# Performance work log

Hardware: AMD Instinct MI355X
Metric: run time of the kernel (lower is better)

The kernel has to match this reference:

```python
import jax, jax.numpy as jnp
import numpy as np

D_MODEL, N_HEADS = 512, 8
HEAD_DIM = D_MODEL // N_HEADS
LN_EPS = 1e-5


def setup_inputs() -> dict:
    key = jax.random.key(0)
    ks = jax.random.split(key, 6)
    b, n = 8, 1024
    x = jax.random.normal(ks[0], (b, n, D_MODEL), dtype=jnp.float32)
    W_qkv = jax.random.normal(ks[1], (D_MODEL, 3 * D_MODEL), dtype=jnp.float32) * (1.0 / np.sqrt(D_MODEL))
    b_qkv = jnp.zeros((3 * D_MODEL,), dtype=jnp.float32)
    reattn_w = jax.random.normal(ks[2], (N_HEADS, N_HEADS), dtype=jnp.float32)
    ln_g = jnp.ones((N_HEADS,), dtype=jnp.float32)
    ln_b = jnp.zeros((N_HEADS,), dtype=jnp.float32)
    W_out = jax.random.normal(ks[3], (D_MODEL, D_MODEL), dtype=jnp.float32) * (1.0 / np.sqrt(D_MODEL))
    b_out = jnp.zeros((D_MODEL,), dtype=jnp.float32)
    return {"x": x, "W_qkv": W_qkv, "b_qkv": b_qkv, "reattn_w": reattn_w,
            "ln_g": ln_g, "ln_b": ln_b, "W_out": W_out, "b_out": b_out}


def reference(x, W_qkv, b_qkv, reattn_w, ln_g, ln_b, W_out, b_out):
    b, n, _ = x.shape
    scale = jnp.float32(HEAD_DIM ** -0.5)  # lsa=False -> non-trainable constant
    qkv = x @ W_qkv + b_qkv                                  # (b, n, 3*d_model)
    q, k, v = jnp.split(qkv, 3, axis=-1)
    def to_heads(t):  # b n (h d) -> b h n d
        return t.reshape(b, n, N_HEADS, HEAD_DIM).transpose(0, 2, 1, 3)
    q, k, v = to_heads(q), to_heads(k), to_heads(v)
    scores = jnp.einsum('bhid,bhjd->bhij', q, k) * scale      # (b, h, n, n)
    attn = jax.nn.softmax(scores, axis=-1)
    # cross-head re-attention mix
    attn = jnp.einsum('bhij,hk->bkij', attn, reattn_w)
    # LayerNorm over the head axis (axis=1)
    mu = jnp.mean(attn, axis=1, keepdims=True)
    var = jnp.var(attn, axis=1, keepdims=True)
    attn = (attn - mu) * jax.lax.rsqrt(var + LN_EPS)
    attn = attn * ln_g[None, :, None, None] + ln_b[None, :, None, None]
    out = jnp.einsum('bhij,bhjd->bhid', attn, v)              # (b, h, n, d)
    out = out.transpose(0, 2, 1, 3).reshape(b, n, D_MODEL)    # b n (h d)
    out = out @ W_out + b_out
    return (out, attn)
```

## Files before the change

### kernel.cpp

```cpp
#include <hip/hip_runtime.h>
#include <hip/hip_bf16.h>

#define SCALE_ 0.125f
#define LN_EPS_ 1e-5f

typedef __attribute__((ext_vector_type(8))) short bf16x8;
typedef __attribute__((ext_vector_type(4))) float f32x4;

__device__ __forceinline__ ushort f2b(float f) {
  union { float f; unsigned u; } x; x.f = f;
  unsigned r = x.u + 0x7FFFu + ((x.u >> 16) & 1u);
  return (ushort)(r >> 16);
}
__device__ __forceinline__ unsigned cvtpk(float lo, float hi) {
  union { __hip_bfloat162 h; unsigned u; } x;
  x.h = __float22bfloat162_rn(make_float2(lo, hi));
  return x.u;
}

__device__ __forceinline__ f32x4 mfma16(bf16x8 a, bf16x8 b, f32x4 c) {
  return __builtin_amdgcn_mfma_f32_16x16x32_bf16(a, b, c, 0, 0, 0);
}

__device__ __forceinline__ void bar_lds() {
  asm volatile("s_waitcnt lgkmcnt(0)\n\ts_barrier" ::: "memory");
  __builtin_amdgcn_sched_barrier(0);
}

__global__ __launch_bounds__(256) void cast_transpose(const float* __restrict__ src,
                                                      ushort* __restrict__ dst,
                                                      int R, int C) {
  __shared__ ushort t[64][65];
  const int tid = threadIdx.x;
  const int c0 = blockIdx.x * 64, r0 = blockIdx.y * 64;
  const int lr = tid >> 2, lc = (tid & 3) * 16;
#pragma unroll
  for (int u = 0; u < 4; ++u) {
    float4 v = *(const float4*)&src[(size_t)(r0 + lr) * C + c0 + lc + u * 4];
    t[lc + u * 4 + 0][lr] = f2b(v.x);
    t[lc + u * 4 + 1][lr] = f2b(v.y);
    t[lc + u * 4 + 2][lr] = f2b(v.z);
    t[lc + u * 4 + 3][lr] = f2b(v.w);
  }
  __syncthreads();
#pragma unroll
  for (int u = 0; u < 2; ++u) {
    bf16x8 o;
#pragma unroll
    for (int e = 0; e < 8; ++e) o[e] = (short)t[lr][lc + u * 8 + e];
    *(bf16x8*)&dst[(size_t)(c0 + lr) * R + r0 + lc + u * 8] = o;
  }
}

__global__ __launch_bounds__(256) void qkv_mfma(const float* __restrict__ x,
                                                const ushort* __restrict__ Wt,
                                                const float* __restrict__ bias,
                                                ushort* __restrict__ q,
                                                ushort* __restrict__ k,
                                                ushort* __restrict__ vt) {
  __shared__ ushort A[128][40];
  __shared__ ushort Bs[128][40];
  const int tid = threadIdx.x;
  const int n0 = blockIdx.x * 128;
  const int m0 = blockIdx.y * 128;
  const int lane = tid & 63, wid = tid >> 6;
  const int wr = wid >> 1, wc = wid & 1;
  const int lr = lane & 15, g4 = lane >> 4;
  const int sr = tid >> 1, sco = (tid & 1) * 16;
  f32x4 acc[4][4] = {};
  for (int k0 = 0; k0 < 512; k0 += 32) {
    {
      const float4* xs = (const float4*)&x[(size_t)(m0 + sr) * 512 + k0 + sco];
      float4 v0 = xs[0], v1 = xs[1], v2 = xs[2], v3 = xs[3];
      bf16x8 p0, p1;
      p0[0] = (short)f2b(v0.x); p0[1] = (short)f2b(v0.y);
      p0[2] = (short)f2b(v0.z); p0[3] = (short)f2b(v0.w);
      p0[4] = (short)f2b(v1.x); p0[5] = (short)f2b(v1.y);
      p0[6] = (short)f2b(v1.z); p0[7] = (short)f2b(v1.w);
      p1[0] = (short)f2b(v2.x); p1[1] = (short)f2b(v2.y);
      p1[2] = (short)f2b(v2.z); p1[3] = (short)f2b(v2.w);
      p1[4] = (short)f2b(v3.x); p1[5] = (short)f2b(v3.y);
      p1[6] = (short)f2b(v3.z); p1[7] = (short)f2b(v3.w);
      *(bf16x8*)&A[sr][sco] = p0;
      *(bf16x8*)&A[sr][sco + 8] = p1;
    }
    {
      const bf16x8* wp = (const bf16x8*)&Wt[(size_t)(n0 + sr) * 512 + k0 + sco];
      *(bf16x8*)&Bs[sr][sco] = wp[0];
      *(bf16x8*)&Bs[sr][sco + 8] = wp[1];
    }
    __syncthreads();
    bf16x8 af[4], bf[4];
#pragma unroll
    for (int mr = 0; mr < 4; ++mr) af[mr] = *(bf16x8*)&A[wr * 64 + mr * 16 + lr][g4 * 8];
#pragma unroll
    for (int nr = 0; nr < 4; ++nr) bf[nr] = *(bf16x8*)&Bs[wc * 64 + nr * 16 + lr][g4 * 8];
#pragma unroll
    for (int mr = 0; mr < 4; ++mr)
#pragma unroll
      for (int nr = 0; nr < 4; ++nr) acc[mr][nr] = mfma16(af[mr], bf[nr], acc[mr][nr]);
    __syncthreads();
  }
  const int part = n0 >> 9;
#pragma unroll
  for (int mr = 0; mr < 4; ++mr)
#pragma unroll
    for (int nr = 0; nr < 4; ++nr) {
      const int n = n0 + wc * 64 + nr * 16 + lr;
      const int h = (n & 511) >> 6, d = n & 63;
      const float bb = bias[n];
#pragma unroll
      for (int r = 0; r < 4; ++r) {
        int token = m0 + wr * 64 + mr * 16 + g4 * 4 + r;
        int bi = token >> 10, ii = token & 1023;
        ushort valb = f2b(acc[mr][nr][r] + bb);
        if (part == 0)
          q[(((size_t)(bi * 8 + h) * 1024 + ii) * 64) + d] = valb;
        else if (part == 1)
          k[(((size_t)(bi * 8 + h) * 1024 + ii) * 64) + d] = valb;
        else
          vt[((size_t)(bi * 8 + h) * 64 + d) * 1024 + ii] = valb;
      }
    }
}

__global__ __launch_bounds__(512, 2) void attn_fused(const ushort* __restrict__ q,
                                                     const ushort* __restrict__ k,
                                                     const ushort* __restrict__ vt,
                                                     const float* __restrict__ rw,
                                                     const float* __restrict__ ln_g,
                                                     const float* __restrict__ ln_b,
                                                     float* __restrict__ attn,
                                                     ushort* __restrict__ pv) {
  __shared__ float PM[8][32][36];
  __shared__ float wsh[64];
  __shared__ float gsh[8], bsh[8];

  const int tid = threadIdx.x;
  const int lane = tid & 63;
  const int h = tid >> 6;
  const int obid = ((blockIdx.x & 7) << 5) + (blockIdx.x >> 3);
  const int i0 = (obid & 31) * 32;
  const int b = obid >> 5;
  const int lr = lane & 15, g4 = lane >> 4;

  const int bh = b * 8 + h;
  const ushort* qh = q + ((size_t)bh * 1024 + i0) * 64;
  const ushort* kh = k + (size_t)bh * 65536;
  const ushort* vth = vt + (size_t)bh * 65536;

  if (tid < 64) wsh[tid] = rw[tid];
  if (tid < 8) { gsh[tid] = ln_g[tid]; bsh[tid] = ln_b[tid]; }

  bf16x8 qf[2][2];
#pragma unroll
  for (int ir = 0; ir < 2; ++ir)
#pragma unroll
    for (int ks = 0; ks < 2; ++ks)
      qf[ir][ks] = *(const bf16x8*)&qh[(size_t)(ir * 16 + lr) * 64 + ks * 32 + g4 * 8];

  float psum[2] = {0.f, 0.f};
  {
    bf16x8 kc[4], kn[4];
#pragma unroll
    for (int jr = 0; jr < 2; ++jr)
#pragma unroll
      for (int ks = 0; ks < 2; ++ks)
        kc[jr * 2 + ks] = *(const bf16x8*)&kh[(size_t)(jr * 16 + lr) * 64 + ks * 32 + g4 * 8];
    for (int jt = 0; jt < 32; ++jt) {
      const int j0n = ((jt + 1) & 31) * 32;
#pragma unroll
      for (int jr = 0; jr < 2; ++jr)
#pragma unroll
        for (int ks = 0; ks < 2; ++ks)
          kn[jr * 2 + ks] =
              *(const bf16x8*)&kh[(size_t)(j0n + jr * 16 + lr) * 64 + ks * 32 + g4 * 8];
      f32x4 sa[2][2] = {};
#pragma unroll
      for (int jr = 0; jr < 2; ++jr)
#pragma unroll
        for (int ir = 0; ir < 2; ++ir) {
          sa[jr][ir] = mfma16(kc[jr * 2 + 0], qf[ir][0], sa[jr][ir]);
          sa[jr][ir] = mfma16(kc[jr * 2 + 1], qf[ir][1], sa[jr][ir]);
        }
#pragma unroll
      for (int jr = 0; jr < 2; ++jr)
#pragma unroll
        for (int ir = 0; ir < 2; ++ir)
#pragma unroll
          for (int r = 0; r < 4; ++r) psum[ir] += __expf(sa[jr][ir][r] * SCALE_);
#pragma unroll
      for (int i = 0; i < 4; ++i) kc[i] = kn[i];
    }
  }
  float inv_[2];
#pragma unroll
  for (int ir = 0; ir < 2; ++ir) {
    float s = psum[ir];
    s += __shfl_xor(s, 16);
    s += __shfl_xor(s, 32);
    inv_[ir] = 1.0f / s;
  }

  f32x4 oaccT[4][2] = {};
  const int pair = tid & 1, chunk = tid >> 1;
  const int m_ii = chunk >> 3, m_jj = (chunk & 7) * 4;
  const int k2base = pair * 4;

  bf16x8 kc[4], kn[4];
#pragma unroll
  for (int jr = 0; jr < 2; ++jr)
#pragma unroll
    for (int ks = 0; ks < 2; ++ks)
      kc[jr * 2 + ks] = *(const bf16x8*)&kh[(size_t)(jr * 16 + lr) * 64 + ks * 32 + g4 * 8];

  for (int jt = 0; jt < 32; ++jt) {
    const int j0 = jt * 32;
    const int j0n = ((jt + 1) & 31) * 32;
#pragma unroll
    for (int jr = 0; jr < 2; ++jr)
#pragma unroll
      for (int ks = 0; ks < 2; ++ks)
        kn[jr * 2 + ks] =
            *(const bf16x8*)&kh[(size_t)(j0n + jr * 16 + lr) * 64 + ks * 32 + g4 * 8];

    f32x4 sa[2][2] = {};
#pragma unroll
    for (int jr = 0; jr < 2; ++jr)
#pragma unroll
      for (int ir = 0; ir < 2; ++ir) {
        sa[jr][ir] = mfma16(kc[jr * 2 + 0], qf[ir][0], sa[jr][ir]);
        sa[jr][ir] = mfma16(kc[jr * 2 + 1], qf[ir][1], sa[jr][ir]);
      }
#pragma unroll
    for (int jr = 0; jr < 2; ++jr)
#pragma unroll
      for (int ir = 0; ir < 2; ++ir) {
        f32x4 pw;
#pragma unroll
        for (int r = 0; r < 4; ++r) pw[r] = __expf(sa[jr][ir][r] * SCALE_) * inv_[ir];
        *(f32x4*)&PM[h][ir * 16 + lr][jr * 16 + g4 * 4] = pw;
      }

    bf16x8 vc[4];
#pragma unroll
    for (int dr = 0; dr < 4; ++dr)
      vc[dr] = *(const bf16x8*)&vth[(size_t)(dr * 16 + lr) * 1024 + j0 + g4 * 8];

    bar_lds();

    float4 ph[8];
#pragma unroll
    for (int h2 = 0; h2 < 8; ++h2) ph[h2] = *(const float4*)&PM[h2][m_ii][m_jj];
    float mixed[4][4];
#pragma unroll
    for (int k2l = 0; k2l < 4; ++k2l) {
      float a0 = 0.f, a1 = 0.f, a2 = 0.f, a3 = 0.f;
#pragma unroll
      for (int h2 = 0; h2 < 8; ++h2) {
        float w = wsh[h2 * 8 + k2base + k2l];
        a0 += ph[h2].x * w; a1 += ph[h2].y * w;
        a2 += ph[h2].z * w; a3 += ph[h2].w * w;
      }
      mixed[k2l][0] = a0; mixed[k2l][1] = a1; mixed[k2l][2] = a2; mixed[k2l][3] = a3;
    }
    float mu[4], rs_[4];
#pragma unroll
    for (int e = 0; e < 4; ++e) {
      float mp = mixed[0][e] + mixed[1][e] + mixed[2][e] + mixed[3][e];
      mu[e] = (mp + __shfl_xor(mp, 1)) * 0.125f;
    }
#pragma unroll
    for (int e = 0; e < 4; ++e) {
      float vp = 0.f;
#pragma unroll
      for (int k2l = 0; k2l < 4; ++k2l) {
        float d = mixed[k2l][e] - mu[e];
        vp += d * d;
      }
      float var = (vp + __shfl_xor(vp, 1)) * 0.125f;
      rs_[e] = rsqrtf(var + LN_EPS_);
    }
#pragma unroll
    for (int k2l = 0; k2l < 4; ++k2l) {
      int k2 = k2base + k2l;
      float g = gsh[k2], be = bsh[k2];
      f32x4 o;
      o[0] = (mixed[k2l][0] - mu[0]) * rs_[0] * g + be;
      o[1] = (mixed[k2l][1] - mu[1]) * rs_[1] * g + be;
      o[2] = (mixed[k2l][2] - mu[2]) * rs_[2] * g + be;
      o[3] = (mixed[k2l][3] - mu[3]) * rs_[3] * g + be;
      __builtin_nontemporal_store(
          o, (f32x4*)&attn[((size_t)(b * 8 + k2) << 20) + ((size_t)(i0 + m_ii) << 10) +
                           j0 + m_jj]);
      *(f32x4*)&PM[k2][m_ii][m_jj] = o;
    }

    bar_lds();

    bf16x8 pab[2];
#pragma unroll
    for (int ic = 0; ic < 2; ++ic) {
      const float* pr = &PM[h][ic * 16 + lr][g4 * 8];
      float4 p0 = *(const float4*)&pr[0];
      float4 p1 = *(const float4*)&pr[4];
      union { bf16x8 v; unsigned u[4]; } pk;
      pk.u[0] = cvtpk(p0.x, p0.y);
      pk.u[1] = cvtpk(p0.z, p0.w);
      pk.u[2] = cvtpk(p1.x, p1.y);
      pk.u[3] = cvtpk(p1.z, p1.w);
      pab[ic] = pk.v;
    }
#pragma unroll
    for (int dr = 0; dr < 4; ++dr) {
      oaccT[dr][0] = mfma16(vc[dr], pab[0], oaccT[dr][0]);
      oaccT[dr][1] = mfma16(vc[dr], pab[1], oaccT[dr][1]);
    }

#pragma unroll
    for (int i = 0; i < 4; ++i) kc[i] = kn[i];
  }

  ushort* po = pv + ((size_t)bh * 1024 + i0) * 64;
#pragma unroll
  for (int ic = 0; ic < 2; ++ic)
#pragma unroll
    for (int dr = 0; dr < 4; ++dr) {
      union { ushort4 s; unsigned u[2]; } o;
      o.u[0] = cvtpk(oaccT[dr][ic][0], oaccT[dr][ic][1]);
      o.u[1] = cvtpk(oaccT[dr][ic][2], oaccT[dr][ic][3]);
      *(ushort4*)&po[(size_t)(ic * 16 + lr) * 64 + dr * 16 + g4 * 4] = o.s;
    }
}

__global__ __launch_bounds__(256) void out_mfma(const ushort* __restrict__ pvb,
                                                const ushort* __restrict__ Wt,
                                                const float* __restrict__ bias,
                                                float* __restrict__ out) {
  __shared__ ushort A[128][40];
  __shared__ ushort Bs[128][40];
  const int tid = threadIdx.x;
  const int n0 = blockIdx.x * 128;
  const int m0 = blockIdx.y * 128;
  const int lane = tid & 63, wid = tid >> 6;
  const int wr = wid >> 1, wc = wid & 1;
  const int lr = lane & 15, g4 = lane >> 4;
  const int sr = tid >> 1, sco = (tid & 1) * 16;
  f32x4 acc[4][4] = {};
  for (int k0 = 0; k0 < 512; k0 += 32) {
    {
      int token = m0 + sr;
      int bi = token >> 10, ii = token & 1023;
      int f = k0 + sco;
      int hh = f >> 6, d = f & 63;
      const bf16x8* src =
          (const bf16x8*)&pvb[(((size_t)(bi * 8 + hh)) * 1024 + ii) * 64 + d];
      *(bf16x8*)&A[sr][sco] = src[0];
      *(bf16x8*)&A[sr][sco + 8] = src[1];
    }
    {
      const bf16x8* wp = (const bf16x8*)&Wt[(size_t)(n0 + sr) * 512 + k0 + sco];
      *(bf16x8*)&Bs[sr][sco] = wp[0];
      *(bf16x8*)&Bs[sr][sco + 8] = wp[1];
    }
    __syncthreads();
    bf16x8 af[4], bf[4];
#pragma unroll
    for (int mr = 0; mr < 4; ++mr) af[mr] = *(bf16x8*)&A[wr * 64 + mr * 16 + lr][g4 * 8];
#pragma unroll
    for (int nr = 0; nr < 4; ++nr) bf[nr] = *(bf16x8*)&Bs[wc * 64 + nr * 16 + lr][g4 * 8];
#pragma unroll
    for (int mr = 0; mr < 4; ++mr)
#pragma unroll
      for (int nr = 0; nr < 4; ++nr) acc[mr][nr] = mfma16(af[mr], bf[nr], acc[mr][nr]);
    __syncthreads();
  }
#pragma unroll
  for (int mr = 0; mr < 4; ++mr)
#pragma unroll
    for (int nr = 0; nr < 4; ++nr) {
      const int n = n0 + wc * 64 + nr * 16 + lr;
      const float bb = bias[n];
#pragma unroll
      for (int r = 0; r < 4; ++r) {
        int token = m0 + wr * 64 + mr * 16 + g4 * 4 + r;
        out[(size_t)token * 512 + n] = acc[mr][nr][r] + bb;
      }
    }
}

extern "C" void kernel_launch(void* const* d_in, const int* in_sizes, int n_in,
                              void* d_out, int out_size, void* d_ws, size_t ws_size,
                              hipStream_t stream) {
  const float* x    = (const float*)d_in[0];
  const float* Wqkv = (const float*)d_in[1];
  const float* bqkv = (const float*)d_in[2];
  const float* rw   = (const float*)d_in[3];
  const float* lng  = (const float*)d_in[4];
  const float* lnb  = (const float*)d_in[5];
  const float* Wout = (const float*)d_in[6];
  const float* bout = (const float*)d_in[7];

  float* out  = (float*)d_out;
  float* attn = (float*)d_out + 4194304;

  char* wsb = (char*)d_ws;
  ushort* q     = (ushort*)(wsb);
  ushort* k     = (ushort*)(wsb + (8u << 20));
  ushort* vt    = (ushort*)(wsb + (16u << 20));
  ushort* pvb   = (ushort*)(wsb + (24u << 20));
  ushort* Wqkvt = (ushort*)(wsb + (32u << 20));
  ushort* Woutt = (ushort*)(wsb + (33u << 20) + (1u << 19));

  cast_transpose<<<dim3(24, 8), 256, 0, stream>>>(Wqkv, Wqkvt, 512, 1536);
  cast_transpose<<<dim3(8, 8), 256, 0, stream>>>(Wout, Woutt, 512, 512);

  qkv_mfma<<<dim3(12, 64), 256, 0, stream>>>(x, Wqkvt, bqkv, q, k, vt);
  attn_fused<<<dim3(256), 512, 0, stream>>>(q, k, vt, rw, lng, lnb, attn, pvb);
  out_mfma<<<dim3(4, 64), 256, 0, stream>>>(pvb, Woutt, bout, out);
}
```

Measured before the change: 185.0 us.

## Double-buffer LDS score tiles to drop one barrier per attention step

The shared score/mix buffer is split into two halves, and the loop is software-pipelined. Each iteration computes scores for tile jt into one buffer while the PV matmul for tile jt-1 reads the other, leaving one LDS barrier per iteration instead of two. The aim is to cut block-wide sync stalls and let MFMA work overlap the mixing and LayerNorm phase. It doubles LDS use for this buffer, which could lower occupancy, and adds a prologue and epilogue.

```diff
diff --git a/kernel.cpp b/kernel.cpp
--- a/kernel.cpp
+++ b/kernel.cpp
@@ -132,7 +132,7 @@
                                                      const float* __restrict__ ln_b,
                                                      float* __restrict__ attn,
                                                      ushort* __restrict__ pv) {
-  __shared__ float PM[8][32][36];
+  __shared__ float PMraw[2][8][32][36];
   __shared__ float wsh[64];
   __shared__ float gsh[8], bsh[8];
 
@@ -161,27 +161,27 @@
 
   float psum[2] = {0.f, 0.f};
   {
-    bf16x8 kc[4], kn[4];
+    bf16x8 kc0[4], kn0[4];
 #pragma unroll
     for (int jr = 0; jr < 2; ++jr)
 #pragma unroll
       for (int ks = 0; ks < 2; ++ks)
-        kc[jr * 2 + ks] = *(const bf16x8*)&kh[(size_t)(jr * 16 + lr) * 64 + ks * 32 + g4 * 8];
+        kc0[jr * 2 + ks] = *(const bf16x8*)&kh[(size_t)(jr * 16 + lr) * 64 + ks * 32 + g4 * 8];
     for (int jt = 0; jt < 32; ++jt) {
       const int j0n = ((jt + 1) & 31) * 32;
 #pragma unroll
       for (int jr = 0; jr < 2; ++jr)
 #pragma unroll
         for (int ks = 0; ks < 2; ++ks)
-          kn[jr * 2 + ks] =
+          kn0[jr * 2 + ks] =
               *(const bf16x8*)&kh[(size_t)(j0n + jr * 16 + lr) * 64 + ks * 32 + g4 * 8];
       f32x4 sa[2][2] = {};
 #pragma unroll
       for (int jr = 0; jr < 2; ++jr)
 #pragma unroll
         for (int ir = 0; ir < 2; ++ir) {
-          sa[jr][ir] = mfma16(kc[jr * 2 + 0], qf[ir][0], sa[jr][ir]);
-          sa[jr][ir] = mfma16(kc[jr * 2 + 1], qf[ir][1], sa[jr][ir]);
+          sa[jr][ir] = mfma16(kc0[jr * 2 + 0], qf[ir][0], sa[jr][ir]);
+          sa[jr][ir] = mfma16(kc0[jr * 2 + 1], qf[ir][1], sa[jr][ir]);
         }
 #pragma unroll
       for (int jr = 0; jr < 2; ++jr)
@@ -190,7 +190,7 @@
 #pragma unroll
           for (int r = 0; r < 4; ++r) psum[ir] += __expf(sa[jr][ir][r] * SCALE_);
 #pragma unroll
-      for (int i = 0; i < 4; ++i) kc[i] = kn[i];
+      for (int i = 0; i < 4; ++i) kc0[i] = kn0[i];
     }
   }
   float inv_[2];
@@ -202,6 +202,10 @@
     inv_[ir] = 1.0f / s;
   }
 
+  typedef float pmhead[32][36];
+  pmhead* PS = (pmhead*)PMraw[0];
+  pmhead* PP = (pmhead*)PMraw[1];
+
   f32x4 oaccT[4][2] = {};
   const int pair = tid & 1, chunk = tid >> 1;
   const int m_ii = chunk >> 3, m_jj = (chunk & 7) * 4;
@@ -214,111 +218,119 @@
     for (int ks = 0; ks < 2; ++ks)
       kc[jr * 2 + ks] = *(const bf16x8*)&kh[(size_t)(jr * 16 + lr) * 64 + ks * 32 + g4 * 8];
 
-  for (int jt = 0; jt < 32; ++jt) {
+#define S_PHASE(JT)                                                                   \
+  {                                                                                   \
+    const int j0n_ = (((JT) + 1) & 31) * 32;                                          \
+    _Pragma("unroll") for (int jr = 0; jr < 2; ++jr)                                  \
+        _Pragma("unroll") for (int ks = 0; ks < 2; ++ks)                              \
+            kn[jr * 2 + ks] = *(const bf16x8*)&kh[(size_t)(j0n_ + jr * 16 + lr) * 64 + \
+                                                  ks * 32 + g4 * 8];                  \
+    f32x4 sa[2][2] = {};                                                              \
+    _Pragma("unroll") for (int jr = 0; jr < 2; ++jr)                                  \
+        _Pragma("unroll") for (int ir = 0; ir < 2; ++ir) {                            \
+      sa[jr][ir] = mfma16(kc[jr * 2 + 0], qf[ir][0], sa[jr][ir]);                     \
+      sa[jr][ir] = mfma16(kc[jr * 2 + 1], qf[ir][1], sa[jr][ir]);                     \
+    }                                                                                 \
+    _Pragma("unroll") for (int jr = 0; jr < 2; ++jr)                                  \
+        _Pragma("unroll") for (int ir = 0; ir < 2; ++ir) {                            \
+      f32x4 pw;                                                                       \
+      _Pragma("unroll") for (int r = 0; r < 4; ++r)                                   \
+          pw[r] = __expf(sa[jr][ir][r] * SCALE_) * inv_[ir];                          \
+      *(f32x4*)&PS[h][ir * 16 + lr][jr * 16 + g4 * 4] = pw;                           \
+    }                                                                                 \
+    _Pragma("unroll") for (int i = 0; i < 4; ++i) kc[i] = kn[i];                      \
+  }
+
+#define MIX_PHASE(J0)                                                                 \
+  {                                                                                   \
+    float4 ph[8];                                                                     \
+    _Pragma("unroll") for (int h2 = 0; h2 < 8; ++h2)                                  \
+        ph[h2] = *(const float4*)&PS[h2][m_ii][m_jj];                                 \
+    float mixed[4][4];                                                                \
+    _Pragma("unroll") for (int k2l = 0; k2l < 4; ++k2l) {                             \
+      float a0 = 0.f, a1 = 0.f, a2 = 0.f, a3 = 0.f;                                   \
+      _Pragma("unroll") for (int h2 = 0; h2 < 8; ++h2) {                              \
+        float w = wsh[h2 * 8 + k2base + k2l];                                         \
+        a0 += ph[h2].x * w; a1 += ph[h2].y * w;                                       \
+        a2 += ph[h2].z * w; a3 += ph[h2].w * w;                                       \
+      }                                                                               \
+      mixed[k2l][0] = a0; mixed[k2l][1] = a1;                                         \
+      mixed[k2l][2] = a2; mixed[k2l][3] = a3;                                         \
+    }                                                                                 \
+    float mu[4], rs_[4];                                                              \
+    _Pragma("unroll") for (int e = 0; e < 4; ++e) {                                   \
+      float mp = mixed[0][e] + mixed[1][e] + mixed[2][e] + mixed[3][e];               \
+      mu[e] = (mp + __shfl_xor(mp, 1)) * 0.125f;                                      \
+    }                                                                                 \
+    _Pragma("unroll") for (int e = 0; e < 4; ++e) {                                   \
+      float vp = 0.f;                                                                 \
+      _Pragma("unroll") for (int k2l = 0; k2l < 4; ++k2l) {                           \
+        float d = mixed[k2l][e] - mu[e];                                              \
+        vp += d * d;                                                                  \
+      }                                                                               \
+      float var = (vp + __shfl_xor(vp, 1)) * 0.125f;                                  \
+      rs_[e] = rsqrtf(var + LN_EPS_);                                                 \
+    }                                                                                 \
+    _Pragma("unroll") for (int k2l = 0; k2l < 4; ++k2l) {                             \
+      int k2 = k2base + k2l;                                                          \
+      float g = gsh[k2], be = bsh[k2];                                                \
+      f32x4 o;                                                                        \
+      o[0] = (mixed[k2l][0] - mu[0]) * rs_[0] * g + be;                               \
+      o[1] = (mixed[k2l][1] - mu[1]) * rs_[1] * g + be;                               \
+      o[2] = (mixed[k2l][2] - mu[2]) * rs_[2] * g + be;                               \
+      o[3] = (mixed[k2l][3] - mu[3]) * rs_[3] * g + be;                               \
+      __builtin_nontemporal_store(                                                    \
+          o, (f32x4*)&attn[((size_t)(b * 8 + k2) << 20) +                             \
+                           ((size_t)(i0 + m_ii) << 10) + (J0) + m_jj]);               \
+      *(f32x4*)&PS[k2][m_ii][m_jj] = o;                                               \
+    }                                                                                 \
+  }
+
+#define PV_PHASE()                                                                    \
+  {                                                                                   \
+    bf16x8 pab[2];                                                                    \
+    _Pragma("unroll") for (int ic = 0; ic < 2; ++ic) {                                \
+      const float* pr = &PP[h][ic * 16 + lr][g4 * 8];                                 \
+      float4 p0 = *(const float4*)&pr[0];                                             \
+      float4 p1 = *(const float4*)&pr[4];                                             \
+      union { bf16x8 v; unsigned u[4]; } pk;                                          \
+      pk.u[0] = cvtpk(p0.x, p0.y);                                                    \
+      pk.u[1] = cvtpk(p0.z, p0.w);                                                    \
+      pk.u[2] = cvtpk(p1.x, p1.y);                                                    \
+      pk.u[3] = cvtpk(p1.z, p1.w);                                                    \
+      pab[ic] = pk.v;                                                                 \
+    }                                                                                 \
+    _Pragma("unroll") for (int dr = 0; dr < 4; ++dr) {                                \
+      oaccT[dr][0] = mfma16(vc[dr], pab[0], oaccT[dr][0]);                            \
+      oaccT[dr][1] = mfma16(vc[dr], pab[1], oaccT[dr][1]);                            \
+    }                                                                                 \
+  }
+
+  S_PHASE(0);
+  bar_lds();
+  MIX_PHASE(0);
+  { pmhead* t = PS; PS = PP; PP = t; }
+
+  for (int jt = 1; jt < 32; ++jt) {
     const int j0 = jt * 32;
-    const int j0n = ((jt + 1) & 31) * 32;
-#pragma unroll
-    for (int jr = 0; jr < 2; ++jr)
-#pragma unroll
-      for (int ks = 0; ks < 2; ++ks)
-        kn[jr * 2 + ks] =
-            *(const bf16x8*)&kh[(size_t)(j0n + jr * 16 + lr) * 64 + ks * 32 + g4 * 8];
-
-    f32x4 sa[2][2] = {};
-#pragma unroll
-    for (int jr = 0; jr < 2; ++jr)
-#pragma unroll
-      for (int ir = 0; ir < 2; ++ir) {
-        sa[jr][ir] = mfma16(kc[jr * 2 + 0], qf[ir][0], sa[jr][ir]);
-        sa[jr][ir] = mfma16(kc[jr * 2 + 1], qf[ir][1], sa[jr][ir]);
-      }
-#pragma unroll
-    for (int jr = 0; jr < 2; ++jr)
-#pragma unroll
-      for (int ir = 0; ir < 2; ++ir) {
-        f32x4 pw;
-#pragma unroll
-        for (int r = 0; r < 4; ++r) pw[r] = __expf(sa[jr][ir][r] * SCALE_) * inv_[ir];
-        *(f32x4*)&PM[h][ir * 16 + lr][jr * 16 + g4 * 4] = pw;
-      }
-
+    S_PHASE(jt);
     bf16x8 vc[4];
 #pragma unroll
     for (int dr = 0; dr < 4; ++dr)
-      vc[dr] = *(const bf16x8*)&vth[(size_t)(dr * 16 + lr) * 1024 + j0 + g4 * 8];
-
+      vc[dr] = *(const bf16x8*)&vth[(size_t)(dr * 16 + lr) * 1024 + (j0 - 32) + g4 * 8];
     bar_lds();
-
-    float4 ph[8];
-#pragma unroll
-    for (int h2 = 0; h2 < 8; ++h2) ph[h2] = *(const float4*)&PM[h2][m_ii][m_jj];
-    float mixed[4][4];
-#pragma unroll
-    for (int k2l = 0; k2l < 4; ++k2l) {
-      float a0 = 0.f, a1 = 0.f, a2 = 0.f, a3 = 0.f;
-#pragma unroll
-      for (int h2 = 0; h2 < 8; ++h2) {
-        float w = wsh[h2 * 8 + k2base + k2l];
-        a0 += ph[h2].x * w; a1 += ph[h2].y * w;
-        a2 += ph[h2].z * w; a3 += ph[h2].w * w;
-      }
-      mixed[k2l][0] = a0; mixed[k2l][1] = a1; mixed[k2l][2] = a2; mixed[k2l][3] = a3;
-    }
-    float mu[4], rs_[4];
-#pragma unroll
-    for (int e = 0; e < 4; ++e) {
-      float mp = mixed[0][e] + mixed[1][e] + mixed[2][e] + mixed[3][e];
-      mu[e] = (mp + __shfl_xor(mp, 1)) * 0.125f;
-    }
-#pragma unroll
-    for (int e = 0; e < 4; ++e) {
-      float vp = 0.f;
-#pragma unroll
-      for (int k2l = 0; k2l < 4; ++k2l) {
-        float d = mixed[k2l][e] - mu[e];
-        vp += d * d;
-      }
-      float var = (vp + __shfl_xor(vp, 1)) * 0.125f;
-      rs_[e] = rsqrtf(var + LN_EPS_);
-    }
-#pragma unroll
-    for (int k2l = 0; k2l < 4; ++k2l) {
-      int k2 = k2base + k2l;
-      float g = gsh[k2], be = bsh[k2];
-      f32x4 o;
-      o[0] = (mixed[k2l][0] - mu[0]) * rs_[0] * g + be;
-      o[1] = (mixed[k2l][1] - mu[1]) * rs_[1] * g + be;
-      o[2] = (mixed[k2l][2] - mu[2]) * rs_[2] * g + be;
-      o[3] = (mixed[k2l][3] - mu[3]) * rs_[3] * g + be;
-      __builtin_nontemporal_store(
-          o, (f32x4*)&attn[((size_t)(b * 8 + k2) << 20) + ((size_t)(i0 + m_ii) << 10) +
-                           j0 + m_jj]);
-      *(f32x4*)&PM[k2][m_ii][m_jj] = o;
-    }
-
+    MIX_PHASE(j0);
+    PV_PHASE();
+    { pmhead* t = PS; PS = PP; PP = t; }
+  }
+
+  {
+    bf16x8 vc[4];
+#pragma unroll
+    for (int dr = 0; dr < 4; ++dr)
+      vc[dr] = *(const bf16x8*)&vth[(size_t)(dr * 16 + lr) * 1024 + 992 + g4 * 8];
     bar_lds();
-
-    bf16x8 pab[2];
-#pragma unroll
-    for (int ic = 0; ic < 2; ++ic) {
-      const float* pr = &PM[h][ic * 16 + lr][g4 * 8];
-      float4 p0 = *(const float4*)&pr[0];
-      float4 p1 = *(const float4*)&pr[4];
-      union { bf16x8 v; unsigned u[4]; } pk;
-      pk.u[0] = cvtpk(p0.x, p0.y);
-      pk.u[1] = cvtpk(p0.z, p0.w);
-      pk.u[2] = cvtpk(p1.x, p1.y);
-      pk.u[3] = cvtpk(p1.z, p1.w);
-      pab[ic] = pk.v;
-    }
-#pragma unroll
-    for (int dr = 0; dr < 4; ++dr) {
-      oaccT[dr][0] = mfma16(vc[dr], pab[0], oaccT[dr][0]);
-      oaccT[dr][1] = mfma16(vc[dr], pab[1], oaccT[dr][1]);
-    }
-
-#pragma unroll
-    for (int i = 0; i < 4; ++i) kc[i] = kn[i];
+    PV_PHASE();
   }
 
   ushort* po = pv + ((size_t)bh * 1024 + i0) * 64;
@@ -331,6 +343,9 @@
       o.u[1] = cvtpk(oaccT[dr][ic][2], oaccT[dr][ic][3]);
       *(ushort4*)&po[(size_t)(ic * 16 + lr) * 64 + dr * 16 + g4 * 4] = o.s;
     }
+#undef S_PHASE
+#undef MIX_PHASE
+#undef PV_PHASE
 }
 
 __global__ __launch_bounds__(256) void out_mfma(const ushort* __restrict__ pvb,
```

After: 189.5 us. 1.02x slower.

## Split softmax denominator pass into separate small-block kernel

Applied to the files above, without the earlier changes.

Moves the first pass that computes softmax row sums (QK^T plus exp) out of the 512-thread fused attention kernel into a new 2048-block, 64-thread kernel that writes reciprocals to workspace. The fused kernel then only loads these reciprocals. The aim is better occupancy and load balance for the denominator pass, since the fused kernel has only 256 blocks. The cost is an extra launch, a small global round trip, and reloading Q/K in a separate kernel.

```diff
diff --git a/kernel.cpp b/kernel.cpp
--- a/kernel.cpp
+++ b/kernel.cpp
@@ -124,12 +124,77 @@
     }
 }
 
+__global__ __launch_bounds__(64) void denoms(const ushort* __restrict__ q,
+                                             const ushort* __restrict__ k,
+                                             float* __restrict__ invg) {
+  const int bid = blockIdx.x;
+  const int obid = ((bid & 7) << 8) + (bid >> 3);
+  const int bh = obid >> 5;
+  const int it = obid & 31;
+  const int lane = threadIdx.x;
+  const int lr = lane & 15, g4 = lane >> 4;
+  const ushort* qh = q + ((size_t)bh * 1024 + it * 32) * 64;
+  const ushort* kh = k + (size_t)bh * 65536;
+
+  bf16x8 qf[2][2];
+#pragma unroll
+  for (int ir = 0; ir < 2; ++ir)
+#pragma unroll
+    for (int ks = 0; ks < 2; ++ks)
+      qf[ir][ks] = *(const bf16x8*)&qh[(size_t)(ir * 16 + lr) * 64 + ks * 32 + g4 * 8];
+
+  float psum[2] = {0.f, 0.f};
+  bf16x8 kc[4], kn[4];
+#pragma unroll
+  for (int jr = 0; jr < 2; ++jr)
+#pragma unroll
+    for (int ks = 0; ks < 2; ++ks)
+      kc[jr * 2 + ks] = *(const bf16x8*)&kh[(size_t)(jr * 16 + lr) * 64 + ks * 32 + g4 * 8];
+  for (int jt = 0; jt < 32; ++jt) {
+    const int j0n = ((jt + 1) & 31) * 32;
+#pragma unroll
+    for (int jr = 0; jr < 2; ++jr)
+#pragma unroll
+      for (int ks = 0; ks < 2; ++ks)
+        kn[jr * 2 + ks] =
+            *(const bf16x8*)&kh[(size_t)(j0n + jr * 16 + lr) * 64 + ks * 32 + g4 * 8];
+    f32x4 sa[2][2] = {};
+#pragma unroll
+    for (int jr = 0; jr < 2; ++jr)
+#pragma unroll
+      for (int ir = 0; ir < 2; ++ir) {
+        sa[jr][ir] = mfma16(kc[jr * 2 + 0], qf[ir][0], sa[jr][ir]);
+        sa[jr][ir] = mfma16(kc[jr * 2 + 1], qf[ir][1], sa[jr][ir]);
+      }
+#pragma unroll
+    for (int jr = 0; jr < 2; ++jr)
+#pragma unroll
+      for (int ir = 0; ir < 2; ++ir)
+#pragma unroll
+        for (int r = 0; r < 4; ++r) psum[ir] += __expf(sa[jr][ir][r] * SCALE_);
+#pragma unroll
+    for (int i = 0; i < 4; ++i) kc[i] = kn[i];
+  }
+#pragma unroll
+  for (int ir = 0; ir < 2; ++ir) {
+    float s = psum[ir];
+    s += __shfl_xor(s, 16);
+    s += __shfl_xor(s, 32);
+    psum[ir] = s;
+  }
+  if (lane < 16) {
+    invg[(size_t)bh * 1024 + it * 32 + lr] = 1.0f / psum[0];
+    invg[(size_t)bh * 1024 + it * 32 + 16 + lr] = 1.0f / psum[1];
+  }
+}
+
 __global__ __launch_bounds__(512, 2) void attn_fused(const ushort* __restrict__ q,
                                                      const ushort* __restrict__ k,
                                                      const ushort* __restrict__ vt,
                                                      const float* __restrict__ rw,
                                                      const float* __restrict__ ln_g,
                                                      const float* __restrict__ ln_b,
+                                                     const float* __restrict__ invg,
                                                      float* __restrict__ attn,
                                                      ushort* __restrict__ pv) {
   __shared__ float PM[8][32][36];
@@ -159,48 +224,10 @@
     for (int ks = 0; ks < 2; ++ks)
       qf[ir][ks] = *(const bf16x8*)&qh[(size_t)(ir * 16 + lr) * 64 + ks * 32 + g4 * 8];
 
-  float psum[2] = {0.f, 0.f};
-  {
-    bf16x8 kc[4], kn[4];
-#pragma unroll
-    for (int jr = 0; jr < 2; ++jr)
-#pragma unroll
-      for (int ks = 0; ks < 2; ++ks)
-        kc[jr * 2 + ks] = *(const bf16x8*)&kh[(size_t)(jr * 16 + lr) * 64 + ks * 32 + g4 * 8];
-    for (int jt = 0; jt < 32; ++jt) {
-      const int j0n = ((jt + 1) & 31) * 32;
-#pragma unroll
-      for (int jr = 0; jr < 2; ++jr)
-#pragma unroll
-        for (int ks = 0; ks < 2; ++ks)
-          kn[jr * 2 + ks] =
-              *(const bf16x8*)&kh[(size_t)(j0n + jr * 16 + lr) * 64 + ks * 32 + g4 * 8];
-      f32x4 sa[2][2] = {};
-#pragma unroll
-      for (int jr = 0; jr < 2; ++jr)
-#pragma unroll
-        for (int ir = 0; ir < 2; ++ir) {
-          sa[jr][ir] = mfma16(kc[jr * 2 + 0], qf[ir][0], sa[jr][ir]);
-          sa[jr][ir] = mfma16(kc[jr * 2 + 1], qf[ir][1], sa[jr][ir]);
-        }
-#pragma unroll
-      for (int jr = 0; jr < 2; ++jr)
-#pragma unroll
-        for (int ir = 0; ir < 2; ++ir)
-#pragma unroll
-          for (int r = 0; r < 4; ++r) psum[ir] += __expf(sa[jr][ir][r] * SCALE_);
-#pragma unroll
-      for (int i = 0; i < 4; ++i) kc[i] = kn[i];
-    }
-  }
   float inv_[2];
 #pragma unroll
-  for (int ir = 0; ir < 2; ++ir) {
-    float s = psum[ir];
-    s += __shfl_xor(s, 16);
-    s += __shfl_xor(s, 32);
-    inv_[ir] = 1.0f / s;
-  }
+  for (int ir = 0; ir < 2; ++ir)
+    inv_[ir] = invg[(size_t)bh * 1024 + i0 + ir * 16 + lr];
 
   f32x4 oaccT[4][2] = {};
   const int pair = tid & 1, chunk = tid >> 1;
@@ -411,11 +438,13 @@
   ushort* pvb   = (ushort*)(wsb + (24u << 20));
   ushort* Wqkvt = (ushort*)(wsb + (32u << 20));
   ushort* Woutt = (ushort*)(wsb + (33u << 20) + (1u << 19));
+  float*  invg  = (float*)(wsb + (34u << 20));
 
   cast_transpose<<<dim3(24, 8), 256, 0, stream>>>(Wqkv, Wqkvt, 512, 1536);
   cast_transpose<<<dim3(8, 8), 256, 0, stream>>>(Wout, Woutt, 512, 512);
 
   qkv_mfma<<<dim3(12, 64), 256, 0, stream>>>(x, Wqkvt, bqkv, q, k, vt);
-  attn_fused<<<dim3(256), 512, 0, stream>>>(q, k, vt, rw, lng, lnb, attn, pvb);
+  denoms<<<dim3(2048), 64, 0, stream>>>(q, k, invg);
+  attn_fused<<<dim3(256), 512, 0, stream>>>(q, k, vt, rw, lng, lnb, invg, attn, pvb);
   out_mfma<<<dim3(4, 64), 256, 0, stream>>>(pvb, Woutt, bout, out);
 }
```

Result: no change. 186.2 us (+0.7%).
